# Kernel tuning notes

Measured on AMD Instinct MI355X. Metric: run time of the kernel, lower is better.

## Reference

```python
import jax, jax.numpy as jnp
import numpy as np

D = 2048      # hidden_size
H = 16        # num_heads
DH = D // H   # head_dim
DFF = 8192    # intermediate_size
EPS = 1e-6


def setup_inputs() -> dict:
    key = jax.random.key(0)
    ks = jax.random.split(key, 12)
    s = 0.02
    return {
        "x": jax.random.normal(ks[0], (2, 2048, D), dtype=jnp.float32),
        "wq": jax.random.normal(ks[1], (D, D), dtype=jnp.float32) * s,
        "bq": jnp.zeros((D,), dtype=jnp.float32),
        "wk": jax.random.normal(ks[2], (D, D), dtype=jnp.float32) * s,
        "bk": jnp.zeros((D,), dtype=jnp.float32),
        "wv": jax.random.normal(ks[3], (D, D), dtype=jnp.float32) * s,
        "bv": jnp.zeros((D,), dtype=jnp.float32),
        "wo": jax.random.normal(ks[4], (D, D), dtype=jnp.float32) * s,
        "bo": jnp.zeros((D,), dtype=jnp.float32),
        "w_gate": jax.random.normal(ks[5], (DFF, D), dtype=jnp.float32) * s,
        "w_up": jax.random.normal(ks[6], (DFF, D), dtype=jnp.float32) * s,
        "w_down": jax.random.normal(ks[7], (D, DFF), dtype=jnp.float32) * s,
        "g_att": jnp.ones((D,), dtype=jnp.float32),
        "g_ffn": jnp.ones((D,), dtype=jnp.float32),
    }


def _rmsnorm(x, w):
    # Faithful to source: multiplies by sqrt(mean(x^2)+eps) (source bug kept).
    var = jnp.mean(x * x, axis=-1, keepdims=True)
    return x * jnp.sqrt(var + EPS) * w


def _mha(x, wq, bq, wk, bk, wv, bv, wo, bo):
    B, S, _ = x.shape
    def split(t):  # [B,S,D] -> [B,H,S,DH]
        return t.reshape(B, S, H, DH).transpose(0, 2, 1, 3)
    q = split(x @ wq.T + bq)
    k = split(x @ wk.T + bk)
    v = split(x @ wv.T + bv)
    scores = jnp.einsum("bhsd,bhtd->bhst", q, k) / jnp.sqrt(jnp.float32(DH))
    probs = jax.nn.softmax(scores, axis=-1)
    out = jnp.einsum("bhst,bhtd->bhsd", probs, v)       # [B,H,S,DH]
    # Faithful quirk: transpose(-1,-2) (NOT (1,2)), then view(B,-1,D)
    out = out.transpose(0, 1, 3, 2).reshape(B, S, D)    # scrambled layout, as in source
    return out @ wo.T + bo


def _ffn(x, w_gate, w_up, w_down):
    inter = jax.nn.relu(x @ w_gate.T) * (x @ w_up.T)
    return inter @ w_down.T


def reference(x, wq, bq, wk, bk, wv, bv, wo, bo, w_gate, w_up, w_down, g_att, g_ffn):
    h = x + _mha(_rmsnorm(x, g_att), wq, bq, wk, bk, wv, bv, wo, bo)
    out = h + _ffn(_rmsnorm(h, g_ffn), w_gate, w_up, w_down)
    return out
```

## Files before the change

### kernel.cpp

```cpp
#include <hip/hip_runtime.h>

typedef __attribute__((ext_vector_type(8))) short short8;
typedef __attribute__((ext_vector_type(4))) float f32x4;
typedef __attribute__((ext_vector_type(4))) unsigned short us4;
typedef unsigned short u16;

__device__ __forceinline__ u16 f2bf(float f) {
    unsigned u = __builtin_bit_cast(unsigned, f);
    return (u16)((u + 0x7fffu + ((u >> 16) & 1u)) >> 16);
}
__device__ __forceinline__ float bf2f(u16 h) {
    unsigned u = ((unsigned)h) << 16;
    return __builtin_bit_cast(float, u);
}
__device__ __forceinline__ void async16(const void* g, void* l) {
    __builtin_amdgcn_global_load_lds((const __attribute__((address_space(1))) unsigned int*)g,
                                     (__attribute__((address_space(3))) unsigned int*)l,
                                     16, 0, 0);
}

__global__ __launch_bounds__(256) void cvt_k(const float* __restrict__ in, u16* __restrict__ out) {
    int i = (blockIdx.x * 256 + threadIdx.x) * 4;
    f32x4 v = *(const f32x4*)(in + i);
    us4 o;
    o[0] = f2bf(v[0]); o[1] = f2bf(v[1]); o[2] = f2bf(v[2]); o[3] = f2bf(v[3]);
    *(us4*)(out + i) = o;
}

__global__ __launch_bounds__(256) void rmsnorm_k(const float* __restrict__ X, const float* __restrict__ g,
                                                 u16* __restrict__ O) {
    const int row = blockIdx.x, tid = threadIdx.x;
    const float* xr = X + (long)row * 2048 + tid * 8;
    f32x4 v0 = *(const f32x4*)xr;
    f32x4 v1 = *(const f32x4*)(xr + 4);
    float ss = v0[0]*v0[0] + v0[1]*v0[1] + v0[2]*v0[2] + v0[3]*v0[3]
             + v1[0]*v1[0] + v1[1]*v1[1] + v1[2]*v1[2] + v1[3]*v1[3];
#pragma unroll
    for (int m = 1; m < 64; m <<= 1) ss += __shfl_xor(ss, m, 64);
    __shared__ float wsum[4];
    if ((tid & 63) == 0) wsum[tid >> 6] = ss;
    __syncthreads();
    float tot = wsum[0] + wsum[1] + wsum[2] + wsum[3];
    const float sc = sqrtf(tot * (1.0f / 2048.0f) + 1e-6f);
    const float* gr = g + tid * 8;
    f32x4 g0 = *(const f32x4*)gr, g1 = *(const f32x4*)(gr + 4);
    us4 o0, o1;
    o0[0] = f2bf(v0[0] * sc * g0[0]); o0[1] = f2bf(v0[1] * sc * g0[1]);
    o0[2] = f2bf(v0[2] * sc * g0[2]); o0[3] = f2bf(v0[3] * sc * g0[3]);
    o1[0] = f2bf(v1[0] * sc * g1[0]); o1[1] = f2bf(v1[1] * sc * g1[1]);
    o1[2] = f2bf(v1[2] * sc * g1[2]); o1[3] = f2bf(v1[3] * sc * g1[3]);
    u16* op = O + (long)row * 2048 + tid * 8;
    *(us4*)op = o0;
    *(us4*)(op + 4) = o1;
}

enum { M_QKV = 0, M_VT = 1, M_H1 = 2, M_RELU = 3, M_MUL = 4, M_ADD = 5 };

template <int MODE, int BN>
__global__ __launch_bounds__(512, 2) void gemm8p(const u16* __restrict__ A, const u16* __restrict__ W,
                                                 const float* __restrict__ bias, const float* resid,
                                                 const u16* aux, void* out,
                                                 int N, int K, float scale) {
    constexpr int MF = BN / 32;
    constexpr int HF = 4;
    constexpr int NF = 4;
    constexpr int BSLOT = BN * 32;
    __shared__ alignas(16) u16 As[2][2][8192];
    __shared__ alignas(16) u16 Bs[2][2][BSLOT];

    const int tid = threadIdx.x, wv = tid >> 6, lane = tid & 63;
    const int q4 = lane >> 4, lr = lane & 15;
    const int wm = (BN == 256) ? (wv >> 2) * 128 : (wv >> 1) * 64;
    const int wn = (BN == 256) ? (wv & 3) * 64 : (wv & 1) * 64;

    const int ntn = N / BN;
    int wg = blockIdx.x;
    {
        const int nwg = gridDim.x, q = nwg >> 3, r = nwg & 7, x = wg & 7, l = wg >> 3;
        wg = (x < r ? x * (q + 1) : r * (q + 1) + (x - r) * q) + l;
    }
    const long m0 = (long)(wg / ntn) * 256;
    const int n0 = (wg % ntn) * BN;

    const int cswz = (q4 ^ ((lr >> 1) & 3)) * 8;
    const int a_rd = (wm + lr) * 32 + cswz;
    const int b_rd = (wn + lr) * 32 + cswz;

    const int srow = tid >> 2;
    const int slc = ((tid & 3) ^ ((srow >> 1) & 3)) * 8;
    const u16* gA0 = A + (m0 + srow) * (long)K + slc;
    const u16* gA1 = gA0 + 128 * (long)K;
    const u16* gB0 = W + ((long)n0 + srow) * K + slc;
    const u16* gB1 = (BN == 256) ? gB0 + 128 * (long)K : gB0;

    f32x4 acc[MF][NF] = {};
    short8 bfr[NF];

#define STAGEA(BUF, KS, KOFF) do {                       \
        u16* d_ = &As[BUF][KS][wv * 512];                \
        async16(gA0 + (KOFF), d_);                       \
        async16(gA1 + (KOFF), d_ + 4096); } while (0)
#define STAGEB(BUF, KS, KOFF) do {                       \
        u16* d_ = &Bs[BUF][KS][wv * 512];                \
        async16(gB0 + (KOFF), d_);                       \
        if (BN == 256) async16(gB1 + (KOFF), d_ + 4096); } while (0)
#define VM(N) asm volatile("s_waitcnt vmcnt(" #N ")")
#define PHASE(BUF, KS, FSEL, RDB, STAGE_, VMW_) do {                                         \
        short8 afr_[HF];                                                                     \
        _Pragma("unroll") for (int m_ = 0; m_ < HF; m_++)                                    \
            afr_[m_] = *(const short8*)(&As[BUF][KS][a_rd + ((FSEL) * HF + m_) * 512]);      \
        if (RDB) {                                                                           \
            _Pragma("unroll") for (int n_ = 0; n_ < NF; n_++)                                \
                bfr[n_] = *(const short8*)(&Bs[BUF][KS][b_rd + n_ * 512]);                   \
        }                                                                                    \
        STAGE_;                                                                              \
        __builtin_amdgcn_s_barrier();                                                        \
        asm volatile("s_waitcnt lgkmcnt(0)");                                                \
        __builtin_amdgcn_s_setprio(1);                                                       \
        _Pragma("unroll") for (int m_ = 0; m_ < HF; m_++)                                    \
            _Pragma("unroll") for (int n_ = 0; n_ < NF; n_++)                                \
                acc[(FSEL) * HF + m_][n_] = __builtin_amdgcn_mfma_f32_16x16x32_bf16(         \
                    afr_[m_], bfr[n_], acc[(FSEL) * HF + m_][n_], 0, 0, 0);                  \
        __builtin_amdgcn_s_setprio(0);                                                       \
        VMW_;                                                                                \
        __builtin_amdgcn_s_barrier();                                                        \
    } while (0)

    const int NI = K >> 7;
    int k0 = 0;

    if constexpr (BN == 256) {
        STAGEB(0, 0, 0);  STAGEA(0, 0, 0);  STAGEB(0, 1, 32); STAGEA(0, 1, 32);
        STAGEB(1, 0, 64); STAGEA(1, 0, 64); STAGEB(1, 1, 96);
        VM(6);
        __builtin_amdgcn_s_barrier();
        for (int i = 0; i < NI - 1; ++i, k0 += 128) {
            PHASE(0, 0, 0, 1, STAGEA(1, 1, k0 + 96),  );
            PHASE(0, 0, 1, 0, STAGEB(0, 0, k0 + 128), );
            PHASE(0, 1, 0, 1, STAGEA(0, 0, k0 + 128), );
            PHASE(0, 1, 1, 0, STAGEB(0, 1, k0 + 160), VM(6));
            PHASE(1, 0, 0, 1, STAGEA(0, 1, k0 + 160), );
            PHASE(1, 0, 1, 0, STAGEB(1, 0, k0 + 192), );
            PHASE(1, 1, 0, 1, STAGEA(1, 0, k0 + 192), );
            PHASE(1, 1, 1, 0, STAGEB(1, 1, k0 + 224), VM(6));
        }
        PHASE(0, 0, 0, 1, STAGEA(1, 1, k0 + 96), );
        PHASE(0, 0, 1, 0, , );
        PHASE(0, 1, 0, 1, , );
        PHASE(0, 1, 1, 0, , VM(0));
        PHASE(1, 0, 0, 1, , );
        PHASE(1, 0, 1, 0, , );
        PHASE(1, 1, 0, 1, , );
        PHASE(1, 1, 1, 0, , );
    } else {
        STAGEB(0, 0, 0);  STAGEA(0, 0, 0);  STAGEB(0, 1, 32); STAGEA(0, 1, 32);
        STAGEB(1, 0, 64); STAGEA(1, 0, 64);
        VM(6);
        __builtin_amdgcn_s_barrier();
        for (int i = 0; i < NI - 1; ++i, k0 += 128) {
            PHASE(0, 0, 0, 1, do { STAGEA(1, 1, k0 + 96);  STAGEB(1, 1, k0 + 96);  } while (0), VM(6));
            PHASE(0, 1, 0, 1, do { STAGEA(0, 0, k0 + 128); STAGEB(0, 0, k0 + 128); } while (0), VM(6));
            PHASE(1, 0, 0, 1, do { STAGEA(0, 1, k0 + 160); STAGEB(0, 1, k0 + 160); } while (0), VM(6));
            PHASE(1, 1, 0, 1, do { STAGEA(1, 0, k0 + 192); STAGEB(1, 0, k0 + 192); } while (0), VM(6));
        }
        PHASE(0, 0, 0, 1, do { STAGEA(1, 1, k0 + 96); STAGEB(1, 1, k0 + 96); } while (0), VM(6));
        PHASE(0, 1, 0, 1, , VM(3));
        PHASE(1, 0, 0, 1, , VM(0));
        PHASE(1, 1, 0, 1, , );
    }

#undef PHASE
#undef VM
#undef STAGEB
#undef STAGEA

#pragma unroll
    for (int m = 0; m < MF; m++) {
#pragma unroll
        for (int n = 0; n < NF; n++) {
            const int gn = n0 + wn + n * 16 + lr;
#pragma unroll
            for (int r = 0; r < 4; r++) {
                const long gm = m0 + wm + m * 16 + q4 * 4 + r;
                float v = acc[m][n][r];
                if constexpr (MODE == M_QKV) {
                    v = (v + bias[gn]) * scale;
                    ((u16*)out)[gm * N + gn] = f2bf(v);
                } else if constexpr (MODE == M_VT) {
                    v = v + bias[gm];
                    const long b = gn >> 11, s = gn & 2047;
                    ((u16*)out)[(b << 22) + gm * 2048 + s] = f2bf(v);
                } else if constexpr (MODE == M_H1) {
                    ((float*)out)[gm * N + gn] = v + bias[gn] + resid[gm * N + gn];
                } else if constexpr (MODE == M_RELU) {
                    ((u16*)out)[gm * N + gn] = f2bf(fmaxf(v, 0.0f));
                } else if constexpr (MODE == M_MUL) {
                    ((u16*)out)[gm * N + gn] = f2bf(v * bf2f(aux[gm * N + gn]));
                } else {
                    ((float*)out)[gm * N + gn] = v + resid[gm * N + gn];
                }
            }
        }
    }
}

__global__ __launch_bounds__(512) void attn_kernel(const u16* __restrict__ Q, const u16* __restrict__ Km,
                                                   const u16* __restrict__ Vt, u16* __restrict__ Oscr) {
    __shared__ u16 Ks[128 * 128];
    __shared__ u16 Vs[128 * 128];
    __shared__ u16 Ps[8][16 * 136];
    __shared__ float abuf[8][16];
    __shared__ float lbuf[8][16];
    const int tid = threadIdx.x, w = tid >> 6, lane = tid & 63;
    const int q4 = lane >> 4, lr = lane & 15;
    const int bh = blockIdx.y, b = bh >> 4, h = bh & 15;
    const int sw = blockIdx.x * 128 + w * 16;
    const long qkbase = ((long)b * 2048) * 2048 + h * 128;
    const long vtbase = ((long)b * 2048 + h * 128) * 2048;

    short8 qf[4];
    {
        const u16* qr = Q + qkbase + (long)(sw + lr) * 2048 + q4 * 8;
#pragma unroll
        for (int kk = 0; kk < 4; kk++) qf[kk] = *(const short8*)(qr + kk * 32);
    }
    float m_i[4], l_i[4];
#pragma unroll
    for (int r = 0; r < 4; r++) { m_i[r] = -1e30f; l_i[r] = 0.0f; }
    f32x4 oacc[8] = {};

    for (int t0 = 0; t0 < 2048; t0 += 128) {
        __syncthreads();
#pragma unroll
        for (int i = 0; i < 4; i++) {
            const int c = i * 512 + tid;
            const int row = c >> 4;
            const int lc = (c & 15) ^ (row & 15);
            async16(Km + qkbase + (long)(t0 + row) * 2048 + lc * 8, (u16*)Ks + (i * 512 + w * 64) * 8);
            async16(Vt + vtbase + (long)row * 2048 + t0 + lc * 8, (u16*)Vs + (i * 512 + w * 64) * 8);
        }
        __syncthreads();
        f32x4 sacc[8] = {};
#pragma unroll
        for (int kk = 0; kk < 4; kk++) {
#pragma unroll
            for (int n = 0; n < 8; n++) {
                const int pc = (kk * 4 + q4) ^ lr;
                short8 kf = *(const short8*)(Ks + ((n * 16 + lr) * 16 + pc) * 8);
                sacc[n] = __builtin_amdgcn_mfma_f32_16x16x32_bf16(qf[kk], kf, sacc[n], 0, 0, 0);
            }
        }
        float al[4];
#pragma unroll
        for (int r = 0; r < 4; r++) {
            float mx = sacc[0][r];
#pragma unroll
            for (int n = 1; n < 8; n++) mx = fmaxf(mx, sacc[n][r]);
#pragma unroll
            for (int msk = 1; msk < 16; msk <<= 1) mx = fmaxf(mx, __shfl_xor(mx, msk, 64));
            const float mn = fmaxf(m_i[r], mx);
            al[r] = __expf(m_i[r] - mn);
            float rs = 0.0f;
#pragma unroll
            for (int n = 0; n < 8; n++) {
                float p = __expf(sacc[n][r] - mn);
                sacc[n][r] = p;
                rs += p;
            }
#pragma unroll
            for (int msk = 1; msk < 16; msk <<= 1) rs += __shfl_xor(rs, msk, 64);
            l_i[r] = l_i[r] * al[r] + rs;
            m_i[r] = mn;
        }
#pragma unroll
        for (int n = 0; n < 8; n++)
#pragma unroll
            for (int r = 0; r < 4; r++)
                Ps[w][(q4 * 4 + r) * 136 + n * 16 + lr] = f2bf(sacc[n][r]);
        if (lr == 0) {
#pragma unroll
            for (int r = 0; r < 4; r++) abuf[w][q4 * 4 + r] = al[r];
        }
        __syncthreads();
        const float a_s = abuf[w][lr];
#pragma unroll
        for (int mm = 0; mm < 8; mm++) oacc[mm] *= a_s;
#pragma unroll
        for (int kk = 0; kk < 4; kk++) {
            short8 pf = *(const short8*)(&Ps[w][lr * 136 + kk * 32 + q4 * 8]);
            const int pc = (kk * 4 + q4) ^ lr;
#pragma unroll
            for (int mm = 0; mm < 8; mm++) {
                short8 vf = *(const short8*)(Vs + ((mm * 16 + lr) * 16 + pc) * 8);
                oacc[mm] = __builtin_amdgcn_mfma_f32_16x16x32_bf16(vf, pf, oacc[mm], 0, 0, 0);
            }
        }
    }
    if (lr == 0) {
#pragma unroll
        for (int r = 0; r < 4; r++) lbuf[w][q4 * 4 + r] = l_i[r];
    }
    __syncthreads();
    const float linv = 1.0f / lbuf[w][lr];
#pragma unroll
    for (int mm = 0; mm < 8; mm++) {
#pragma unroll
        for (int r = 0; r < 4; r++) {
            const int d = mm * 16 + q4 * 4 + r;
            Oscr[vtbase + (long)d * 2048 + sw + lr] = f2bf(oacc[mm][r] * linv);
        }
    }
}

extern "C" void kernel_launch(void* const* d_in, const int* in_sizes, int n_in,
                              void* d_out, int out_size, void* d_ws, size_t ws_size,
                              hipStream_t stream) {
    const float* x  = (const float*)d_in[0];
    const float* wq = (const float*)d_in[1];
    const float* bq = (const float*)d_in[2];
    const float* wk = (const float*)d_in[3];
    const float* bk = (const float*)d_in[4];
    const float* wv = (const float*)d_in[5];
    const float* bv = (const float*)d_in[6];
    const float* wo = (const float*)d_in[7];
    const float* bo = (const float*)d_in[8];
    const float* wg = (const float*)d_in[9];
    const float* wu = (const float*)d_in[10];
    const float* wd = (const float*)d_in[11];
    const float* ga = (const float*)d_in[12];
    const float* gf = (const float*)d_in[13];

    char* ws = (char*)d_ws;
    const size_t MB = (size_t)1 << 20;
    u16*  xn    = (u16*)(ws + 0);
    u16*  scr   = (u16*)(ws + 0);
    u16*  hn    = (u16*)(ws + 0);
    u16*  qb    = (u16*)(ws + 16 * MB);
    u16*  kb    = (u16*)(ws + 32 * MB);
    u16*  vt    = (u16*)(ws + 48 * MB);
    u16*  grelu = (u16*)(ws + 16 * MB);
    u16*  inter = grelu;
    u16*  wreg  = (u16*)(ws + 80 * MB);
    u16*  wq_b  = wreg;
    u16*  wk_b  = wreg + 4 * MB;
    u16*  wv_b  = wreg + 8 * MB;
    u16*  wo_b  = wreg + 12 * MB;
    u16*  wbig  = wreg;
    float* h1   = (float*)d_out;

    cvt_k<<<4096, 256, 0, stream>>>(wq, wq_b);
    cvt_k<<<4096, 256, 0, stream>>>(wk, wk_b);
    cvt_k<<<4096, 256, 0, stream>>>(wv, wv_b);
    cvt_k<<<4096, 256, 0, stream>>>(wo, wo_b);

    rmsnorm_k<<<4096, 256, 0, stream>>>(x, ga, xn);

    const float qscale = 0.08838834764831843f;
    gemm8p<M_QKV, 128><<<256, 512, 0, stream>>>(xn, wq_b, bq, nullptr, nullptr, qb, 2048, 2048, qscale);
    gemm8p<M_QKV, 128><<<256, 512, 0, stream>>>(xn, wk_b, bk, nullptr, nullptr, kb, 2048, 2048, 1.0f);
    gemm8p<M_VT, 128><<<256, 512, 0, stream>>>(wv_b, xn, bv, nullptr, nullptr, vt, 4096, 2048, 1.0f);

    attn_kernel<<<dim3(16, 32), 512, 0, stream>>>(qb, kb, vt, scr);

    gemm8p<M_H1, 128><<<256, 512, 0, stream>>>(scr, wo_b, bo, x, nullptr, h1, 2048, 2048, 1.0f);

    cvt_k<<<16384, 256, 0, stream>>>(wg, wbig);
    rmsnorm_k<<<4096, 256, 0, stream>>>(h1, gf, hn);

    gemm8p<M_RELU, 256><<<512, 512, 0, stream>>>(hn, wbig, nullptr, nullptr, nullptr, grelu, 8192, 2048, 1.0f);

    cvt_k<<<16384, 256, 0, stream>>>(wu, wbig);
    gemm8p<M_MUL, 256><<<512, 512, 0, stream>>>(hn, wbig, nullptr, nullptr, grelu, inter, 8192, 2048, 1.0f);

    cvt_k<<<16384, 256, 0, stream>>>(wd, wbig);
    gemm8p<M_ADD, 128><<<256, 512, 0, stream>>>(inter, wbig, nullptr, h1, nullptr, d_out, 2048, 8192, 1.0f);
}
```

Before: 1.077 ms.

## Double-buffer register fragments to overlap LDS reads with MFMA in GEMM

Restructures the GEMM main loop so LDS fragment reads for the next phase are issued into a second register set before the MFMAs of the current phase. Partial lgkmcnt waits replace the full drain, and the vmcnt waits and barriers are rescheduled to match. This hides LDS read latency behind matrix math. In exchange it uses more VGPRs for the extra A/B fragments, which may hurt occupancy under launch_bounds(512,2), and it relies on hand-tuned wait counts that could race if miscounted.

```diff
diff --git a/kernel.cpp b/kernel.cpp
--- a/kernel.cpp
+++ b/kernel.cpp
@@ -62,7 +62,6 @@
                                                  const u16* aux, void* out,
                                                  int N, int K, float scale) {
     constexpr int MF = BN / 32;
-    constexpr int HF = 4;
     constexpr int NF = 4;
     constexpr int BSLOT = BN * 32;
     __shared__ alignas(16) u16 As[2][2][8192];
@@ -94,7 +93,7 @@
     const u16* gB1 = (BN == 256) ? gB0 + 128 * (long)K : gB0;
 
     f32x4 acc[MF][NF] = {};
-    short8 bfr[NF];
+    short8 afr0[4], afr1[4], bfr0[NF], bfr1[NF];
 
 #define STAGEA(BUF, KS, KOFF) do {                       \
         u16* d_ = &As[BUF][KS][wv * 512];                \
@@ -105,26 +104,21 @@
         async16(gB0 + (KOFF), d_);                       \
         if (BN == 256) async16(gB1 + (KOFF), d_ + 4096); } while (0)
 #define VM(N) asm volatile("s_waitcnt vmcnt(" #N ")")
-#define PHASE(BUF, KS, FSEL, RDB, STAGE_, VMW_) do {                                         \
-        short8 afr_[HF];                                                                     \
-        _Pragma("unroll") for (int m_ = 0; m_ < HF; m_++)                                    \
-            afr_[m_] = *(const short8*)(&As[BUF][KS][a_rd + ((FSEL) * HF + m_) * 512]);      \
-        if (RDB) {                                                                           \
-            _Pragma("unroll") for (int n_ = 0; n_ < NF; n_++)                                \
-                bfr[n_] = *(const short8*)(&Bs[BUF][KS][b_rd + n_ * 512]);                   \
-        }                                                                                    \
-        STAGE_;                                                                              \
-        __builtin_amdgcn_s_barrier();                                                        \
-        asm volatile("s_waitcnt lgkmcnt(0)");                                                \
-        __builtin_amdgcn_s_setprio(1);                                                       \
-        _Pragma("unroll") for (int m_ = 0; m_ < HF; m_++)                                    \
-            _Pragma("unroll") for (int n_ = 0; n_ < NF; n_++)                                \
-                acc[(FSEL) * HF + m_][n_] = __builtin_amdgcn_mfma_f32_16x16x32_bf16(         \
-                    afr_[m_], bfr[n_], acc[(FSEL) * HF + m_][n_], 0, 0, 0);                  \
-        __builtin_amdgcn_s_setprio(0);                                                       \
-        VMW_;                                                                                \
-        __builtin_amdgcn_s_barrier();                                                        \
-    } while (0)
+#define LG(N) asm volatile("s_waitcnt lgkmcnt(" #N ")")
+#define BAR __builtin_amdgcn_s_barrier()
+#define PRDA(SET, BUF, KS, FSEL) do {                                              \
+        _Pragma("unroll") for (int m_ = 0; m_ < 4; m_++)                           \
+            SET[m_] = *(const short8*)(&As[BUF][KS][a_rd + ((FSEL) * 4 + m_) * 512]); } while (0)
+#define PRDB(SET, BUF, KS) do {                                                    \
+        _Pragma("unroll") for (int n_ = 0; n_ < NF; n_++)                          \
+            SET[n_] = *(const short8*)(&Bs[BUF][KS][b_rd + n_ * 512]); } while (0)
+#define MM(AF, BF, RB) do {                                                        \
+        __builtin_amdgcn_s_setprio(1);                                             \
+        _Pragma("unroll") for (int m_ = 0; m_ < 4; m_++)                           \
+            _Pragma("unroll") for (int n_ = 0; n_ < NF; n_++)                      \
+                acc[(RB) + m_][n_] = __builtin_amdgcn_mfma_f32_16x16x32_bf16(      \
+                    AF[m_], BF[n_], acc[(RB) + m_][n_], 0, 0, 0);                  \
+        __builtin_amdgcn_s_setprio(0); } while (0)
 
     const int NI = K >> 7;
     int k0 = 0;
@@ -132,44 +126,50 @@
     if constexpr (BN == 256) {
         STAGEB(0, 0, 0);  STAGEA(0, 0, 0);  STAGEB(0, 1, 32); STAGEA(0, 1, 32);
         STAGEB(1, 0, 64); STAGEA(1, 0, 64); STAGEB(1, 1, 96);
-        VM(6);
-        __builtin_amdgcn_s_barrier();
+        VM(10);
+        BAR;
+        PRDA(afr0, 0, 0, 0); PRDB(bfr0, 0, 0);
         for (int i = 0; i < NI - 1; ++i, k0 += 128) {
-            PHASE(0, 0, 0, 1, STAGEA(1, 1, k0 + 96),  );
-            PHASE(0, 0, 1, 0, STAGEB(0, 0, k0 + 128), );
-            PHASE(0, 1, 0, 1, STAGEA(0, 0, k0 + 128), );
-            PHASE(0, 1, 1, 0, STAGEB(0, 1, k0 + 160), VM(6));
-            PHASE(1, 0, 0, 1, STAGEA(0, 1, k0 + 160), );
-            PHASE(1, 0, 1, 0, STAGEB(1, 0, k0 + 192), );
-            PHASE(1, 1, 0, 1, STAGEA(1, 0, k0 + 192), );
-            PHASE(1, 1, 1, 0, STAGEB(1, 1, k0 + 224), VM(6));
-        }
-        PHASE(0, 0, 0, 1, STAGEA(1, 1, k0 + 96), );
-        PHASE(0, 0, 1, 0, , );
-        PHASE(0, 1, 0, 1, , );
-        PHASE(0, 1, 1, 0, , VM(0));
-        PHASE(1, 0, 0, 1, , );
-        PHASE(1, 0, 1, 0, , );
-        PHASE(1, 1, 0, 1, , );
-        PHASE(1, 1, 1, 0, , );
+            PRDA(afr1, 0, 0, 1);                      STAGEA(1, 1, k0 + 96);  VM(6); LG(4); BAR; MM(afr0, bfr0, 0);
+            PRDA(afr0, 0, 1, 0); PRDB(bfr1, 0, 1);    STAGEB(0, 0, k0 + 128); VM(6); LG(8); BAR; MM(afr1, bfr0, 4);
+            PRDA(afr1, 0, 1, 1);                      STAGEA(0, 0, k0 + 128); VM(6); LG(4); BAR; MM(afr0, bfr1, 0);
+            PRDA(afr0, 1, 0, 0); PRDB(bfr0, 1, 0);    STAGEB(0, 1, k0 + 160); VM(6); LG(8); BAR; MM(afr1, bfr1, 4);
+            PRDA(afr1, 1, 0, 1);                      STAGEA(0, 1, k0 + 160); VM(6); LG(4); BAR; MM(afr0, bfr0, 0);
+            PRDA(afr0, 1, 1, 0); PRDB(bfr1, 1, 1);    STAGEB(1, 0, k0 + 192); VM(6); LG(8); BAR; MM(afr1, bfr0, 4);
+            PRDA(afr1, 1, 1, 1);                      STAGEA(1, 0, k0 + 192); VM(6); LG(4); BAR; MM(afr0, bfr1, 0);
+            PRDA(afr0, 0, 0, 0); PRDB(bfr0, 0, 0);    STAGEB(1, 1, k0 + 224); VM(6); LG(8); BAR; MM(afr1, bfr1, 4);
+        }
+        PRDA(afr1, 0, 0, 1);                      STAGEA(1, 1, k0 + 96); VM(6); LG(4); BAR; MM(afr0, bfr0, 0);
+        PRDA(afr0, 0, 1, 0); PRDB(bfr1, 0, 1);    VM(4); LG(8); BAR; MM(afr1, bfr0, 4);
+        PRDA(afr1, 0, 1, 1);                      VM(2); LG(4); BAR; MM(afr0, bfr1, 0);
+        PRDA(afr0, 1, 0, 0); PRDB(bfr0, 1, 0);    LG(8); BAR; MM(afr1, bfr1, 4);
+        PRDA(afr1, 1, 0, 1);                      VM(0); LG(4); BAR; MM(afr0, bfr0, 0);
+        PRDA(afr0, 1, 1, 0); PRDB(bfr1, 1, 1);    LG(8); BAR; MM(afr1, bfr0, 4);
+        PRDA(afr1, 1, 1, 1);                      LG(4); BAR; MM(afr0, bfr1, 0);
+        LG(0); BAR; MM(afr1, bfr1, 4);
     } else {
         STAGEB(0, 0, 0);  STAGEA(0, 0, 0);  STAGEB(0, 1, 32); STAGEA(0, 1, 32);
         STAGEB(1, 0, 64); STAGEA(1, 0, 64);
-        VM(6);
-        __builtin_amdgcn_s_barrier();
+        VM(3);
+        BAR;
+        PRDA(afr0, 0, 0, 0); PRDB(bfr0, 0, 0);
         for (int i = 0; i < NI - 1; ++i, k0 += 128) {
-            PHASE(0, 0, 0, 1, do { STAGEA(1, 1, k0 + 96);  STAGEB(1, 1, k0 + 96);  } while (0), VM(6));
-            PHASE(0, 1, 0, 1, do { STAGEA(0, 0, k0 + 128); STAGEB(0, 0, k0 + 128); } while (0), VM(6));
-            PHASE(1, 0, 0, 1, do { STAGEA(0, 1, k0 + 160); STAGEB(0, 1, k0 + 160); } while (0), VM(6));
-            PHASE(1, 1, 0, 1, do { STAGEA(1, 0, k0 + 192); STAGEB(1, 0, k0 + 192); } while (0), VM(6));
-        }
-        PHASE(0, 0, 0, 1, do { STAGEA(1, 1, k0 + 96); STAGEB(1, 1, k0 + 96); } while (0), VM(6));
-        PHASE(0, 1, 0, 1, , VM(3));
-        PHASE(1, 0, 0, 1, , VM(0));
-        PHASE(1, 1, 0, 1, , );
-    }
-
-#undef PHASE
+            PRDA(afr1, 0, 1, 0); PRDB(bfr1, 0, 1); STAGEA(1, 1, k0 + 96);  STAGEB(1, 1, k0 + 96);  VM(3); LG(8); BAR; MM(afr0, bfr0, 0);
+            PRDA(afr0, 1, 0, 0); PRDB(bfr0, 1, 0); STAGEA(0, 0, k0 + 128); STAGEB(0, 0, k0 + 128); VM(3); LG(8); BAR; MM(afr1, bfr1, 0);
+            PRDA(afr1, 1, 1, 0); PRDB(bfr1, 1, 1); STAGEA(0, 1, k0 + 160); STAGEB(0, 1, k0 + 160); VM(3); LG(8); BAR; MM(afr0, bfr0, 0);
+            PRDA(afr0, 0, 0, 0); PRDB(bfr0, 0, 0); STAGEA(1, 0, k0 + 192); STAGEB(1, 0, k0 + 192); VM(3); LG(8); BAR; MM(afr1, bfr1, 0);
+        }
+        PRDA(afr1, 0, 1, 0); PRDB(bfr1, 0, 1); STAGEA(1, 1, k0 + 96); STAGEB(1, 1, k0 + 96); VM(3); LG(8); BAR; MM(afr0, bfr0, 0);
+        PRDA(afr0, 1, 0, 0); PRDB(bfr0, 1, 0); VM(0); LG(8); BAR; MM(afr1, bfr1, 0);
+        PRDA(afr1, 1, 1, 0); PRDB(bfr1, 1, 1); LG(8); BAR; MM(afr0, bfr0, 0);
+        LG(0); BAR; MM(afr1, bfr1, 0);
+    }
+
+#undef MM
+#undef PRDB
+#undef PRDA
+#undef BAR
+#undef LG
 #undef VM
 #undef STAGEB
 #undef STAGEA
```

Result: slower. 1.109 ms (+2.9%).
